# Performance work log

Measured on AMD Instinct MI355X. Metric: run time of the kernel, lower is better.

The kernel has to match this reference:

```python
import jax, jax.numpy as jnp
import numpy as np

S = 256          # seq_len
H = 1024         # hidden_size == input_size (required by inputs + hf add)
NUM_ITER = 1     # interaction module inner iterations
EPS = 1e-5       # BatchNorm1d eps


def setup_inputs() -> dict:
    key = jax.random.key(0)
    ks = jax.random.split(key, 16)
    xav = np.sqrt(2.0 / (H + H))          # xavier_normal for HxH dense
    u = 1.0 / np.sqrt(H)                  # torch LSTMCell default init scale
    inp = {"inputs": jax.random.normal(ks[0], (S, H), jnp.float32)}
    # interaction module dense layers
    for i in range(4):
        inp[f"W{i+1}"] = jax.random.normal(ks[1 + i], (H, H), jnp.float32) * xav
        inp[f"b{i+1}"] = jnp.zeros((H,), jnp.float32)
    # LSTM cells (forward / backward)
    inp["Wih_f"] = jax.random.uniform(ks[5], (4 * H, H), jnp.float32, -u, u)
    inp["Whh_f"] = jax.random.uniform(ks[6], (4 * H, H), jnp.float32, -u, u)
    inp["bih_f"] = jax.random.uniform(ks[7], (4 * H,), jnp.float32, -u, u)
    inp["bhh_f"] = jax.random.uniform(ks[8], (4 * H,), jnp.float32, -u, u)
    inp["Wih_b"] = jax.random.uniform(ks[9], (4 * H, H), jnp.float32, -u, u)
    inp["Whh_b"] = jax.random.uniform(ks[10], (4 * H, H), jnp.float32, -u, u)
    inp["bih_b"] = jax.random.uniform(ks[11], (4 * H,), jnp.float32, -u, u)
    inp["bhh_b"] = jax.random.uniform(ks[12], (4 * H,), jnp.float32, -u, u)
    # BatchNorm1d affine params (default init)
    inp["gamma_f"] = jnp.ones((H,), jnp.float32)
    inp["beta_f"] = jnp.zeros((H,), jnp.float32)
    inp["gamma_b"] = jnp.ones((H,), jnp.float32)
    inp["beta_b"] = jnp.zeros((H,), jnp.float32)
    return inp


def _bn(x, g, b):
    # training-mode BatchNorm1d over the batch (seq) axis, biased variance
    m = jnp.mean(x, axis=0)
    xc = x - m
    v = jnp.mean(xc * xc, axis=0)
    return xc * jax.lax.rsqrt(v + EPS) * g + b


def _lstm_c(x, h, c, Wih, Whh, bih, bhh):
    # torch LSTMCell: returns new cell state only (as used by the module)
    g = x @ Wih.T + bih + h @ Whh.T + bhh
    i, f, gg, o = jnp.split(g, 4)
    return jax.nn.sigmoid(f) * c + jax.nn.sigmoid(i) * jnp.tanh(gg)


def reference(inputs, W1, b1, W2, b2, W3, b3, W4, b4,
              Wih_f, Whh_f, bih_f, bhh_f, Wih_b, Whh_b, bih_b, bhh_b,
              gamma_f, beta_f, gamma_b, beta_b):
    sig = jax.nn.sigmoid

    def interaction(x0, hf, hb):
        for _ in range(NUM_ITER):
            x1 = sig((x0 + hf) @ W1.T + b1)
            hb2 = sig((hb + x1) @ W2.T + b2)
            hf2 = sig((x1 + hf) @ W3.T + b3)
            x0 = sig((hb2 + x1) @ W4.T + b4)
            hf, hb = hf2, hb2
        return x0, hf, hb

    def step(carry, t):
        hf, hb, fc, bc = carry
        _, hf2, hb2 = interaction(inputs, hf, hb)
        out = (hf2 + hb2) * 0.5  # value returned at the last timestep (pre-BN)
        tb = S - 1 - t
        fc = fc.at[t].set(_lstm_c(inputs[t], hf2[t], fc[t], Wih_f, Whh_f, bih_f, bhh_f))
        bc = bc.at[tb].set(_lstm_c(inputs[tb], hb2[tb], bc[tb], Wih_b, Whh_b, bih_b, bhh_b))
        hf_n = _bn(hf2, gamma_f, beta_f)
        hb_n = _bn(hb2, gamma_b, beta_b)
        return (hf_n, hb_n, fc, bc), out

    z = jnp.zeros((S, H), jnp.float32)
    (_, _, _, _), outs = jax.lax.scan(step, (z, z, z, z), jnp.arange(S))
    return outs[-1]  # [S, H]
```

## Files before the change

kernel.cpp:

```cpp
#include <hip/hip_runtime.h>
#include <hip/hip_bf16.h>
#include <math.h>

#define S 256
#define H 1024
#define SH (S*H)
#define EPS 1e-5f

typedef float f32x4 __attribute__((ext_vector_type(4)));
typedef short bf16x8 __attribute__((ext_vector_type(8)));

__device__ __forceinline__ float sigm(float x){ return 1.0f/(1.0f+expf(-x)); }

__device__ __forceinline__ ushort f2bf(float a){
    union { __hip_bfloat16 b; ushort u; } cv;
    cv.b = __float2bfloat16(a);
    return cv.u;
}
__device__ __forceinline__ float bf2f(ushort u){
    union { __hip_bfloat16 b; ushort u; } cv; cv.u = u;
    return __bfloat162float(cv.b);
}

__device__ __forceinline__ int xcd_swizzle(unsigned gbx) {
    return (int)((gbx & 7u) * 32u + (gbx >> 3));
}

__global__ __launch_bounds__(256) void k_pack(const float* __restrict__ W,
                                              ushort* __restrict__ ph,
                                              ushort* __restrict__ pl) {
    int p  = blockIdx.x * 256 + threadIdx.x;
    int l  = p & 63;
    int kt = (p >> 6) & 31;
    int jt = p >> 11;
    int j  = jt * 16 + (l & 15);
    int k0 = kt * 32 + ((l >> 4) << 3);
    const float* src = W + j * H + k0;
    float4 a0 = *(const float4*)src;
    float4 a1 = *(const float4*)(src + 4);
    float av[8] = {a0.x,a0.y,a0.z,a0.w,a1.x,a1.y,a1.z,a1.w};
    bf16x8 vh, vl;
#pragma unroll
    for (int e = 0; e < 8; ++e) {
        ushort h = f2bf(av[e]);
        vh[e] = (short)h;
        vl[e] = (short)f2bf(av[e] - bf2f(h));
    }
    *(bf16x8*)(ph + (size_t)p * 8) = vh;
    *(bf16x8*)(pl + (size_t)p * 8) = vl;
}

__global__ __launch_bounds__(256) void k_gemm1(
    const float* __restrict__ X,
    const ushort* __restrict__ Wph, const ushort* __restrict__ Wpl,
    const float* __restrict__ b1v,
    const float* __restrict__ rawF, const float* __restrict__ rawB,
    const float* __restrict__ statPrev,
    const float* __restrict__ gF, const float* __restrict__ bF,
    const float* __restrict__ gB, const float* __restrict__ bB,
    float* __restrict__ A2, float* __restrict__ A3,
    float* __restrict__ statz, int first)
{
    __shared__ __align__(16) ushort lhs_hi[8192];
    __shared__ __align__(16) ushort lhs_lo[8192];
    __shared__ float scF[H], ofF[H];

    int t = threadIdx.x;
    if (blockIdx.x < 16) statz[blockIdx.x * 256 + t] = 0.0f;

    int g = xcd_swizzle(blockIdx.x);
    int sb = g & 7, jb = g >> 3;
    int lane = t & 63, w = t >> 6;
    int wr = w >> 1, wc = w & 1;
    int row0 = sb * 32;
    int jt = jb * 2 + wc;
    const float inv = 1.0f / (float)S;

    if (!first) {
        for (int k = t; k < H; k += 256) {
            float m = statPrev[k] * inv;
            float v = statPrev[H + k] * inv - m * m;
            float sc = rsqrtf(v + EPS) * gF[k];
            scF[k] = sc;
            ofF[k] = bF[k] - m * sc;
        }
    }
    __syncthreads();

    f32x4 acc0 = {0,0,0,0}, acc1 = {0,0,0,0}, acc2 = {0,0,0,0};

    for (int phase = 0; phase < 4; ++phase) {
        int kbase = phase << 8;
#pragma unroll
        for (int it = 0; it < 4; ++it) {
            int gg = t + (it << 8);
            int s  = gg & 31;
            int kg = gg >> 5;
            int k  = kbase + (kg << 3);
            const float* xp = X + (row0 + s) * H + k;
            float4 x0 = *(const float4*)xp;
            float4 x1 = *(const float4*)(xp + 4);
            float a[8] = {x0.x,x0.y,x0.z,x0.w,x1.x,x1.y,x1.z,x1.w};
            if (!first) {
                const float* rp = rawF + (row0 + s) * H + k;
                float4 r0 = *(const float4*)rp;
                float4 r1 = *(const float4*)(rp + 4);
                float rr[8] = {r0.x,r0.y,r0.z,r0.w,r1.x,r1.y,r1.z,r1.w};
#pragma unroll
                for (int e = 0; e < 8; ++e)
                    a[e] += rr[e] * scF[k + e] + ofF[k + e];
            }
            bf16x8 vh, vl;
#pragma unroll
            for (int e = 0; e < 8; ++e) {
                ushort h = f2bf(a[e]);
                vh[e] = (short)h;
                vl[e] = (short)f2bf(a[e] - bf2f(h));
            }
            int st2 = s >> 4, q = kg & 3, kc = kg >> 2;
            int idx = (((st2 * 8 + kc) * 64) + ((q << 4) | (s & 15))) * 8;
            *(bf16x8*)(lhs_hi + idx) = vh;
            *(bf16x8*)(lhs_lo + idx) = vl;
        }
        __syncthreads();
        const ushort* bph = Wph + ((size_t)(jt * 32 + (phase << 3)) * 64 + lane) * 8;
        const ushort* bpl = Wpl + ((size_t)(jt * 32 + (phase << 3)) * 64 + lane) * 8;
        const ushort* ah  = lhs_hi + ((wr * 8) * 64 + lane) * 8;
        const ushort* al  = lhs_lo + ((wr * 8) * 64 + lane) * 8;
#pragma unroll
        for (int kc = 0; kc < 8; ++kc) {
            bf16x8 a_h = *(const bf16x8*)(ah + kc * 512);
            bf16x8 a_l = *(const bf16x8*)(al + kc * 512);
            bf16x8 b_h = *(const bf16x8*)(bph + kc * 512);
            bf16x8 b_l = *(const bf16x8*)(bpl + kc * 512);
            acc0 = __builtin_amdgcn_mfma_f32_16x16x32_bf16(a_h, b_h, acc0, 0, 0, 0);
            acc1 = __builtin_amdgcn_mfma_f32_16x16x32_bf16(a_h, b_l, acc1, 0, 0, 0);
            acc2 = __builtin_amdgcn_mfma_f32_16x16x32_bf16(a_l, b_h, acc2, 0, 0, 0);
        }
        __syncthreads();
    }

    int j = jt * 16 + (lane & 15);
    int srow = row0 + wr * 16 + ((lane >> 4) << 2);
    float bias = b1v[j];
    float scFj = 0.f, ofFj = 0.f, scBj = 0.f, ofBj = 0.f;
    if (!first) {
        scFj = scF[j]; ofFj = ofF[j];
        float m = statPrev[2 * H + j] * inv;
        float v = statPrev[3 * H + j] * inv - m * m;
        scBj = rsqrtf(v + EPS) * gB[j];
        ofBj = bB[j] - m * scBj;
    }
    f32x4 sum = acc0 + acc1 + acc2;
#pragma unroll
    for (int r = 0; r < 4; ++r) {
        int o = (srow + r) * H + j;
        float x1v = sigm(sum[r] + bias);
        float hb_ = first ? 0.f : rawB[o] * scBj + ofBj;
        float hf_ = first ? 0.f : rawF[o] * scFj + ofFj;
        A2[o] = hb_ + x1v;
        A3[o] = x1v + hf_;
    }
}

__global__ __launch_bounds__(256) void k_gemm23(
    const float* __restrict__ A2g, const float* __restrict__ A3g,
    const ushort* __restrict__ W2h, const ushort* __restrict__ W2l,
    const ushort* __restrict__ W3h, const ushort* __restrict__ W3l,
    const float* __restrict__ b2v, const float* __restrict__ b3v,
    float* __restrict__ rawF, float* __restrict__ rawB,
    float* __restrict__ stats, float* __restrict__ outp, int writeOut)
{
    __shared__ __align__(16) ushort lhs_hi[8192];
    __shared__ __align__(16) ushort lhs_lo[8192];
    __shared__ float red[4][64][2];

    int t = threadIdx.x;
    int g = xcd_swizzle(blockIdx.x);
    int sb = g & 7, jb = g >> 3;
    int lane = t & 63, w = t >> 6;
    int wr = w >> 1, wc = w & 1;
    int row0 = sb * 32;
    int jt = jb * 2 + wc;
    int j = jt * 16 + (lane & 15);
    int srow = row0 + wr * 16 + ((lane >> 4) << 2);

    float vb[4];

    {
        f32x4 acc0 = {0,0,0,0}, acc1 = {0,0,0,0}, acc2 = {0,0,0,0};
        for (int phase = 0; phase < 4; ++phase) {
            int kbase = phase << 8;
#pragma unroll
            for (int it = 0; it < 4; ++it) {
                int gg = t + (it << 8);
                int s = gg & 31, kg = gg >> 5;
                int k = kbase + (kg << 3);
                const float* xp = A2g + (row0 + s) * H + k;
                float4 x0 = *(const float4*)xp;
                float4 x1 = *(const float4*)(xp + 4);
                float a[8] = {x0.x,x0.y,x0.z,x0.w,x1.x,x1.y,x1.z,x1.w};
                bf16x8 vh, vl;
#pragma unroll
                for (int e = 0; e < 8; ++e) {
                    ushort h = f2bf(a[e]);
                    vh[e] = (short)h;
                    vl[e] = (short)f2bf(a[e] - bf2f(h));
                }
                int idx = ((((s >> 4) * 8 + (kg >> 2)) * 64) + (((kg & 3) << 4) | (s & 15))) * 8;
                *(bf16x8*)(lhs_hi + idx) = vh;
                *(bf16x8*)(lhs_lo + idx) = vl;
            }
            __syncthreads();
            const ushort* bph = W2h + ((size_t)(jt * 32 + (phase << 3)) * 64 + lane) * 8;
            const ushort* bpl = W2l + ((size_t)(jt * 32 + (phase << 3)) * 64 + lane) * 8;
            const ushort* ah  = lhs_hi + ((wr * 8) * 64 + lane) * 8;
            const ushort* al  = lhs_lo + ((wr * 8) * 64 + lane) * 8;
#pragma unroll
            for (int kc = 0; kc < 8; ++kc) {
                bf16x8 a_h = *(const bf16x8*)(ah + kc * 512);
                bf16x8 a_l = *(const bf16x8*)(al + kc * 512);
                bf16x8 b_h = *(const bf16x8*)(bph + kc * 512);
                bf16x8 b_l = *(const bf16x8*)(bpl + kc * 512);
                acc0 = __builtin_amdgcn_mfma_f32_16x16x32_bf16(a_h, b_h, acc0, 0, 0, 0);
                acc1 = __builtin_amdgcn_mfma_f32_16x16x32_bf16(a_h, b_l, acc1, 0, 0, 0);
                acc2 = __builtin_amdgcn_mfma_f32_16x16x32_bf16(a_l, b_h, acc2, 0, 0, 0);
            }
            __syncthreads();
        }
        f32x4 sum = acc0 + acc1 + acc2;
        float bias = b2v[j];
        float ts = 0.f, tq = 0.f;
#pragma unroll
        for (int r = 0; r < 4; ++r) {
            float v = sigm(sum[r] + bias);
            vb[r] = v;
            rawB[(srow + r) * H + j] = v;
            ts += v; tq += v * v;
        }
        red[w][lane][0] = ts;
        red[w][lane][1] = tq;
    }
    __syncthreads();
    if (t < 32) {
        int wc2 = t >> 4, jl = t & 15;
        int jj = jb * 32 + wc2 * 16 + jl;
        float ts = 0.f, tq = 0.f;
#pragma unroll
        for (int wr2 = 0; wr2 < 2; ++wr2)
#pragma unroll
            for (int lg = 0; lg < 4; ++lg) {
                ts += red[wr2 * 2 + wc2][lg * 16 + jl][0];
                tq += red[wr2 * 2 + wc2][lg * 16 + jl][1];
            }
        atomicAdd(&stats[2 * H + jj], ts);
        atomicAdd(&stats[3 * H + jj], tq);
    }

    {
        f32x4 acc0 = {0,0,0,0}, acc1 = {0,0,0,0}, acc2 = {0,0,0,0};
        for (int phase = 0; phase < 4; ++phase) {
            int kbase = phase << 8;
            __syncthreads();
#pragma unroll
            for (int it = 0; it < 4; ++it) {
                int gg = t + (it << 8);
                int s = gg & 31, kg = gg >> 5;
                int k = kbase + (kg << 3);
                const float* xp = A3g + (row0 + s) * H + k;
                float4 x0 = *(const float4*)xp;
                float4 x1 = *(const float4*)(xp + 4);
                float a[8] = {x0.x,x0.y,x0.z,x0.w,x1.x,x1.y,x1.z,x1.w};
                bf16x8 vh, vl;
#pragma unroll
                for (int e = 0; e < 8; ++e) {
                    ushort h = f2bf(a[e]);
                    vh[e] = (short)h;
                    vl[e] = (short)f2bf(a[e] - bf2f(h));
                }
                int idx = ((((s >> 4) * 8 + (kg >> 2)) * 64) + (((kg & 3) << 4) | (s & 15))) * 8;
                *(bf16x8*)(lhs_hi + idx) = vh;
                *(bf16x8*)(lhs_lo + idx) = vl;
            }
            __syncthreads();
            const ushort* bph = W3h + ((size_t)(jt * 32 + (phase << 3)) * 64 + lane) * 8;
            const ushort* bpl = W3l + ((size_t)(jt * 32 + (phase << 3)) * 64 + lane) * 8;
            const ushort* ah  = lhs_hi + ((wr * 8) * 64 + lane) * 8;
            const ushort* al  = lhs_lo + ((wr * 8) * 64 + lane) * 8;
#pragma unroll
            for (int kc = 0; kc < 8; ++kc) {
                bf16x8 a_h = *(const bf16x8*)(ah + kc * 512);
                bf16x8 a_l = *(const bf16x8*)(al + kc * 512);
                bf16x8 b_h = *(const bf16x8*)(bph + kc * 512);
                bf16x8 b_l = *(const bf16x8*)(bpl + kc * 512);
                acc0 = __builtin_amdgcn_mfma_f32_16x16x32_bf16(a_h, b_h, acc0, 0, 0, 0);
                acc1 = __builtin_amdgcn_mfma_f32_16x16x32_bf16(a_h, b_l, acc1, 0, 0, 0);
                acc2 = __builtin_amdgcn_mfma_f32_16x16x32_bf16(a_l, b_h, acc2, 0, 0, 0);
            }
        }
        __syncthreads();
        f32x4 sum = acc0 + acc1 + acc2;
        float bias = b3v[j];
        float ts = 0.f, tq = 0.f;
#pragma unroll
        for (int r = 0; r < 4; ++r) {
            float v = sigm(sum[r] + bias);
            rawF[(srow + r) * H + j] = v;
            if (writeOut)
                outp[(srow + r) * H + j] = 0.5f * (v + vb[r]);
            ts += v; tq += v * v;
        }
        red[w][lane][0] = ts;
        red[w][lane][1] = tq;
    }
    __syncthreads();
    if (t < 32) {
        int wc2 = t >> 4, jl = t & 15;
        int jj = jb * 32 + wc2 * 16 + jl;
        float ts = 0.f, tq = 0.f;
#pragma unroll
        for (int wr2 = 0; wr2 < 2; ++wr2)
#pragma unroll
            for (int lg = 0; lg < 4; ++lg) {
                ts += red[wr2 * 2 + wc2][lg * 16 + jl][0];
                tq += red[wr2 * 2 + wc2][lg * 16 + jl][1];
            }
        atomicAdd(&stats[0 * H + jj], ts);
        atomicAdd(&stats[1 * H + jj], tq);
    }
}

extern "C" void kernel_launch(void* const* d_in, const int* in_sizes, int n_in,
                              void* d_out, int out_size, void* d_ws, size_t ws_size,
                              hipStream_t stream) {
    (void)in_sizes; (void)n_in; (void)out_size; (void)ws_size;

    const float* X  = (const float*)d_in[0];
    const float* W1 = (const float*)d_in[1];
    const float* b1 = (const float*)d_in[2];
    const float* W2 = (const float*)d_in[3];
    const float* b2 = (const float*)d_in[4];
    const float* W3 = (const float*)d_in[5];
    const float* b3 = (const float*)d_in[6];
    const float* gf = (const float*)d_in[17];
    const float* bf = (const float*)d_in[18];
    const float* gb = (const float*)d_in[19];
    const float* bb = (const float*)d_in[20];

    char* base = (char*)d_ws;
    const size_t MB = 1024 * 1024;
    ushort* wp1h = (ushort*)(base + 0 * MB);
    ushort* wp1l = (ushort*)(base + 2 * MB);
    ushort* wp2h = (ushort*)(base + 4 * MB);
    ushort* wp2l = (ushort*)(base + 6 * MB);
    ushort* wp3h = (ushort*)(base + 8 * MB);
    ushort* wp3l = (ushort*)(base + 10 * MB);
    float*  A2   = (float*)(base + 12 * MB);
    float*  A3   = (float*)(base + 13 * MB);
    float*  rawf = (float*)(base + 14 * MB);
    float*  rawb = (float*)(base + 16 * MB);
    float*  stats= (float*)(base + 18 * MB);

    k_pack<<<512, 256, 0, stream>>>(W1, wp1h, wp1l);
    k_pack<<<512, 256, 0, stream>>>(W2, wp2h, wp2l);
    k_pack<<<512, 256, 0, stream>>>(W3, wp3h, wp3l);

    for (int s = 0; s < S; ++s) {
        int p = (s + 1) & 1;
        int q = s & 1;
        k_gemm1<<<256, 256, 0, stream>>>(
            X, wp1h, wp1l, b1,
            rawf + q * SH, rawb + q * SH, stats + q * 4 * H,
            gf, bf, gb, bb,
            A2, A3, stats + p * 4 * H, (s == 0) ? 1 : 0);
        k_gemm23<<<256, 256, 0, stream>>>(
            A2, A3, wp2h, wp2l, wp3h, wp3l, b2, b3,
            rawf + p * SH, rawb + p * SH, stats + p * 4 * H,
            (float*)d_out, (s == S - 1) ? 1 : 0);
    }
}
```

Before: 14.97 ms.

## Fuse per-step kernels into one persistent kernel with software grid barriers

```diff
diff --git a/kernel.cpp b/kernel.cpp
--- a/kernel.cpp
+++ b/kernel.cpp
@@ -50,283 +50,272 @@
     *(bf16x8*)(pl + (size_t)p * 8) = vl;
 }
 
-__global__ __launch_bounds__(256) void k_gemm1(
+__global__ __launch_bounds__(256) void k_init(float* __restrict__ stats,
+                                              unsigned* __restrict__ sync) {
+    int t = blockIdx.x * 256 + threadIdx.x;
+    if (t < 8 * H) stats[t] = 0.0f;
+    if (t == 0) { sync[0] = 0u; sync[64] = 0u; }
+}
+
+__device__ __forceinline__ void grid_barrier(unsigned* ctrp, unsigned* flagp,
+                                             unsigned want) {
+    __syncthreads();
+    if (threadIdx.x == 0) {
+        __threadfence();
+        unsigned old = __hip_atomic_fetch_add(ctrp, 1u, __ATOMIC_RELAXED,
+                                              __HIP_MEMORY_SCOPE_AGENT);
+        if (old == want * 256u - 1u) {
+            __hip_atomic_store(flagp, want, __ATOMIC_RELEASE,
+                               __HIP_MEMORY_SCOPE_AGENT);
+        } else {
+            while (__hip_atomic_load(flagp, __ATOMIC_RELAXED,
+                                     __HIP_MEMORY_SCOPE_AGENT) < want)
+                __builtin_amdgcn_s_sleep(1);
+        }
+        __threadfence();
+    }
+    __syncthreads();
+}
+
+__global__ __launch_bounds__(256) void k_persist(
     const float* __restrict__ X,
-    const ushort* __restrict__ Wph, const ushort* __restrict__ Wpl,
-    const float* __restrict__ b1v,
-    const float* __restrict__ rawF, const float* __restrict__ rawB,
-    const float* __restrict__ statPrev,
-    const float* __restrict__ gF, const float* __restrict__ bF,
-    const float* __restrict__ gB, const float* __restrict__ bB,
-    float* __restrict__ A2, float* __restrict__ A3,
-    float* __restrict__ statz, int first)
+    const ushort* __restrict__ wp1h, const ushort* __restrict__ wp1l,
+    const ushort* __restrict__ wp2h, const ushort* __restrict__ wp2l,
+    const ushort* __restrict__ wp3h, const ushort* __restrict__ wp3l,
+    const float* __restrict__ b1v, const float* __restrict__ b2v,
+    const float* __restrict__ b3v,
+    const float* __restrict__ gFv, const float* __restrict__ bFv,
+    const float* __restrict__ gBv, const float* __restrict__ bBv,
+    ushort* __restrict__ A2h, ushort* __restrict__ A2l,
+    ushort* __restrict__ A3h, ushort* __restrict__ A3l,
+    float* __restrict__ rawf, float* __restrict__ rawb,
+    float* __restrict__ stats, float* __restrict__ outp,
+    unsigned* __restrict__ syncv)
 {
     __shared__ __align__(16) ushort lhs_hi[8192];
     __shared__ __align__(16) ushort lhs_lo[8192];
     __shared__ float scF[H], ofF[H];
-
-    int t = threadIdx.x;
-    if (blockIdx.x < 16) statz[blockIdx.x * 256 + t] = 0.0f;
-
-    int g = xcd_swizzle(blockIdx.x);
-    int sb = g & 7, jb = g >> 3;
-    int lane = t & 63, w = t >> 6;
-    int wr = w >> 1, wc = w & 1;
-    int row0 = sb * 32;
-    int jt = jb * 2 + wc;
+    __shared__ float red[4][64][2];
+
+    const int t = threadIdx.x;
+    const int g = xcd_swizzle(blockIdx.x);
+    const int sb = g & 7, jb = g >> 3;
+    const int lane = t & 63, w = t >> 6;
+    const int wr = w >> 1, wc = w & 1;
+    const int row0 = sb * 32;
+    const int jt = jb * 2 + wc;
+    const int j = jt * 16 + (lane & 15);
+    const int arow = row0 + wr * 16 + (lane & 15);
+    const int koff = (lane >> 4) << 3;
+    const int srow = row0 + wr * 16 + ((lane >> 4) << 2);
     const float inv = 1.0f / (float)S;
 
-    if (!first) {
-        for (int k = t; k < H; k += 256) {
-            float m = statPrev[k] * inv;
-            float v = statPrev[H + k] * inv - m * m;
-            float sc = rsqrtf(v + EPS) * gF[k];
-            scF[k] = sc;
-            ofF[k] = bF[k] - m * sc;
-        }
-    }
-    __syncthreads();
-
-    f32x4 acc0 = {0,0,0,0}, acc1 = {0,0,0,0}, acc2 = {0,0,0,0};
-
-    for (int phase = 0; phase < 4; ++phase) {
-        int kbase = phase << 8;
-#pragma unroll
-        for (int it = 0; it < 4; ++it) {
-            int gg = t + (it << 8);
-            int s  = gg & 31;
-            int kg = gg >> 5;
-            int k  = kbase + (kg << 3);
-            const float* xp = X + (row0 + s) * H + k;
-            float4 x0 = *(const float4*)xp;
-            float4 x1 = *(const float4*)(xp + 4);
-            float a[8] = {x0.x,x0.y,x0.z,x0.w,x1.x,x1.y,x1.z,x1.w};
+    unsigned* ctrp  = syncv;
+    unsigned* flagp = syncv + 64;
+    unsigned bgen = 0;
+
+    for (int s = 0; s < S; ++s) {
+        const int p = (s + 1) & 1, q = s & 1;
+        const int first = (s == 0);
+        const float* stP = stats + q * 4 * H;
+        float* stA = stats + p * 4 * H;
+        const float* rF = rawf + q * SH;
+        const float* rB = rawb + q * SH;
+        float* wF = rawf + p * SH;
+        float* wB = rawb + p * SH;
+
+        if (!first) {
+            for (int k = t; k < H; k += 256) {
+                float m = stP[k] * inv;
+                float v = stP[H + k] * inv - m * m;
+                float sc = rsqrtf(v + EPS) * gFv[k];
+                scF[k] = sc;
+                ofF[k] = bFv[k] - m * sc;
+            }
+        }
+        __syncthreads();
+
+        {
+            f32x4 acc0 = {0,0,0,0}, acc1 = {0,0,0,0}, acc2 = {0,0,0,0};
+            for (int phase = 0; phase < 4; ++phase) {
+                int kbase = phase << 8;
+#pragma unroll
+                for (int it = 0; it < 4; ++it) {
+                    int gg = t + (it << 8);
+                    int si = gg & 31, kg = gg >> 5;
+                    int k = kbase + (kg << 3);
+                    const float* xp = X + (row0 + si) * H + k;
+                    float4 x0 = *(const float4*)xp;
+                    float4 x1 = *(const float4*)(xp + 4);
+                    float a[8] = {x0.x,x0.y,x0.z,x0.w,x1.x,x1.y,x1.z,x1.w};
+                    if (!first) {
+                        const float* rp = rF + (row0 + si) * H + k;
+                        float4 r0 = *(const float4*)rp;
+                        float4 r1 = *(const float4*)(rp + 4);
+                        float rr[8] = {r0.x,r0.y,r0.z,r0.w,r1.x,r1.y,r1.z,r1.w};
+#pragma unroll
+                        for (int e = 0; e < 8; ++e)
+                            a[e] += rr[e] * scF[k + e] + ofF[k + e];
+                    }
+                    bf16x8 vh, vl;
+#pragma unroll
+                    for (int e = 0; e < 8; ++e) {
+                        ushort h = f2bf(a[e]);
+                        vh[e] = (short)h;
+                        vl[e] = (short)f2bf(a[e] - bf2f(h));
+                    }
+                    int idx = ((((si >> 4) * 8 + (kg >> 2)) * 64) +
+                               (((kg & 3) << 4) | (si & 15))) * 8;
+                    *(bf16x8*)(lhs_hi + idx) = vh;
+                    *(bf16x8*)(lhs_lo + idx) = vl;
+                }
+                __syncthreads();
+                const ushort* bph = wp1h + ((size_t)(jt * 32 + (phase << 3)) * 64 + lane) * 8;
+                const ushort* bpl = wp1l + ((size_t)(jt * 32 + (phase << 3)) * 64 + lane) * 8;
+                const ushort* ah  = lhs_hi + ((wr * 8) * 64 + lane) * 8;
+                const ushort* al  = lhs_lo + ((wr * 8) * 64 + lane) * 8;
+#pragma unroll
+                for (int kc = 0; kc < 8; ++kc) {
+                    bf16x8 a_h = *(const bf16x8*)(ah + kc * 512);
+                    bf16x8 a_l = *(const bf16x8*)(al + kc * 512);
+                    bf16x8 b_h = *(const bf16x8*)(bph + kc * 512);
+                    bf16x8 b_l = *(const bf16x8*)(bpl + kc * 512);
+                    acc0 = __builtin_amdgcn_mfma_f32_16x16x32_bf16(a_h, b_h, acc0, 0, 0, 0);
+                    acc1 = __builtin_amdgcn_mfma_f32_16x16x32_bf16(a_h, b_l, acc1, 0, 0, 0);
+                    acc2 = __builtin_amdgcn_mfma_f32_16x16x32_bf16(a_l, b_h, acc2, 0, 0, 0);
+                }
+                __syncthreads();
+            }
+
+            float bias = b1v[j];
+            float scFj = 0.f, ofFj = 0.f, scBj = 0.f, ofBj = 0.f;
             if (!first) {
-                const float* rp = rawF + (row0 + s) * H + k;
-                float4 r0 = *(const float4*)rp;
-                float4 r1 = *(const float4*)(rp + 4);
-                float rr[8] = {r0.x,r0.y,r0.z,r0.w,r1.x,r1.y,r1.z,r1.w};
-#pragma unroll
-                for (int e = 0; e < 8; ++e)
-                    a[e] += rr[e] * scF[k + e] + ofF[k + e];
-            }
-            bf16x8 vh, vl;
-#pragma unroll
-            for (int e = 0; e < 8; ++e) {
-                ushort h = f2bf(a[e]);
-                vh[e] = (short)h;
-                vl[e] = (short)f2bf(a[e] - bf2f(h));
-            }
-            int st2 = s >> 4, q = kg & 3, kc = kg >> 2;
-            int idx = (((st2 * 8 + kc) * 64) + ((q << 4) | (s & 15))) * 8;
-            *(bf16x8*)(lhs_hi + idx) = vh;
-            *(bf16x8*)(lhs_lo + idx) = vl;
+                scFj = scF[j]; ofFj = ofF[j];
+                float m = stP[2 * H + j] * inv;
+                float v = stP[3 * H + j] * inv - m * m;
+                scBj = rsqrtf(v + EPS) * gBv[j];
+                ofBj = bBv[j] - m * scBj;
+            }
+            f32x4 sum = acc0 + acc1 + acc2;
+#pragma unroll
+            for (int r = 0; r < 4; ++r) {
+                int o = (srow + r) * H + j;
+                float x1v = sigm(sum[r] + bias);
+                float hb_ = first ? 0.f : rB[o] * scBj + ofBj;
+                float hf_ = first ? 0.f : rF[o] * scFj + ofFj;
+                float a2 = hb_ + x1v;
+                float a3 = x1v + hf_;
+                ushort h2 = f2bf(a2);
+                A2h[o] = h2;
+                A2l[o] = f2bf(a2 - bf2f(h2));
+                ushort h3 = f2bf(a3);
+                A3h[o] = h3;
+                A3l[o] = f2bf(a3 - bf2f(h3));
+            }
+        }
+
+        grid_barrier(ctrp, flagp, ++bgen);
+
+        if (blockIdx.x == 0) {
+            float* z = stats + q * 4 * H;
+            for (int k = t; k < 4 * H; k += 256) z[k] = 0.0f;
+        }
+
+        float vb[4];
+        {
+            f32x4 acc0 = {0,0,0,0}, acc1 = {0,0,0,0}, acc2 = {0,0,0,0};
+            const ushort* ah = A2h + arow * H + koff;
+            const ushort* al = A2l + arow * H + koff;
+            const ushort* bh = wp2h + ((size_t)(jt * 32) * 64 + lane) * 8;
+            const ushort* bl = wp2l + ((size_t)(jt * 32) * 64 + lane) * 8;
+#pragma unroll 8
+            for (int kc = 0; kc < 32; ++kc) {
+                bf16x8 vah = *(const bf16x8*)(ah + kc * 32);
+                bf16x8 val = *(const bf16x8*)(al + kc * 32);
+                bf16x8 vbh = *(const bf16x8*)(bh + kc * 512);
+                bf16x8 vbl = *(const bf16x8*)(bl + kc * 512);
+                acc0 = __builtin_amdgcn_mfma_f32_16x16x32_bf16(vah, vbh, acc0, 0, 0, 0);
+                acc1 = __builtin_amdgcn_mfma_f32_16x16x32_bf16(vah, vbl, acc1, 0, 0, 0);
+                acc2 = __builtin_amdgcn_mfma_f32_16x16x32_bf16(val, vbh, acc2, 0, 0, 0);
+            }
+            f32x4 sum = acc0 + acc1 + acc2;
+            float bias = b2v[j];
+            float ts = 0.f, tq = 0.f;
+#pragma unroll
+            for (int r = 0; r < 4; ++r) {
+                float v = sigm(sum[r] + bias);
+                vb[r] = v;
+                wB[(srow + r) * H + j] = v;
+                ts += v; tq += v * v;
+            }
+            red[w][lane][0] = ts;
+            red[w][lane][1] = tq;
         }
         __syncthreads();
-        const ushort* bph = Wph + ((size_t)(jt * 32 + (phase << 3)) * 64 + lane) * 8;
-        const ushort* bpl = Wpl + ((size_t)(jt * 32 + (phase << 3)) * 64 + lane) * 8;
-        const ushort* ah  = lhs_hi + ((wr * 8) * 64 + lane) * 8;
-        const ushort* al  = lhs_lo + ((wr * 8) * 64 + lane) * 8;
-#pragma unroll
-        for (int kc = 0; kc < 8; ++kc) {
-            bf16x8 a_h = *(const bf16x8*)(ah + kc * 512);
-            bf16x8 a_l = *(const bf16x8*)(al + kc * 512);
-            bf16x8 b_h = *(const bf16x8*)(bph + kc * 512);
-            bf16x8 b_l = *(const bf16x8*)(bpl + kc * 512);
-            acc0 = __builtin_amdgcn_mfma_f32_16x16x32_bf16(a_h, b_h, acc0, 0, 0, 0);
-            acc1 = __builtin_amdgcn_mfma_f32_16x16x32_bf16(a_h, b_l, acc1, 0, 0, 0);
-            acc2 = __builtin_amdgcn_mfma_f32_16x16x32_bf16(a_l, b_h, acc2, 0, 0, 0);
+        if (t < 32) {
+            int wc2 = t >> 4, jl = t & 15;
+            int jj = jb * 32 + wc2 * 16 + jl;
+            float ts = 0.f, tq = 0.f;
+#pragma unroll
+            for (int wr2 = 0; wr2 < 2; ++wr2)
+#pragma unroll
+                for (int lg = 0; lg < 4; ++lg) {
+                    ts += red[wr2 * 2 + wc2][lg * 16 + jl][0];
+                    tq += red[wr2 * 2 + wc2][lg * 16 + jl][1];
+                }
+            atomicAdd(&stA[2 * H + jj], ts);
+            atomicAdd(&stA[3 * H + jj], tq);
         }
         __syncthreads();
-    }
-
-    int j = jt * 16 + (lane & 15);
-    int srow = row0 + wr * 16 + ((lane >> 4) << 2);
-    float bias = b1v[j];
-    float scFj = 0.f, ofFj = 0.f, scBj = 0.f, ofBj = 0.f;
-    if (!first) {
-        scFj = scF[j]; ofFj = ofF[j];
-        float m = statPrev[2 * H + j] * inv;
-        float v = statPrev[3 * H + j] * inv - m * m;
-        scBj = rsqrtf(v + EPS) * gB[j];
-        ofBj = bB[j] - m * scBj;
-    }
-    f32x4 sum = acc0 + acc1 + acc2;
-#pragma unroll
-    for (int r = 0; r < 4; ++r) {
-        int o = (srow + r) * H + j;
-        float x1v = sigm(sum[r] + bias);
-        float hb_ = first ? 0.f : rawB[o] * scBj + ofBj;
-        float hf_ = first ? 0.f : rawF[o] * scFj + ofFj;
-        A2[o] = hb_ + x1v;
-        A3[o] = x1v + hf_;
-    }
-}
-
-__global__ __launch_bounds__(256) void k_gemm23(
-    const float* __restrict__ A2g, const float* __restrict__ A3g,
-    const ushort* __restrict__ W2h, const ushort* __restrict__ W2l,
-    const ushort* __restrict__ W3h, const ushort* __restrict__ W3l,
-    const float* __restrict__ b2v, const float* __restrict__ b3v,
-    float* __restrict__ rawF, float* __restrict__ rawB,
-    float* __restrict__ stats, float* __restrict__ outp, int writeOut)
-{
-    __shared__ __align__(16) ushort lhs_hi[8192];
-    __shared__ __align__(16) ushort lhs_lo[8192];
-    __shared__ float red[4][64][2];
-
-    int t = threadIdx.x;
-    int g = xcd_swizzle(blockIdx.x);
-    int sb = g & 7, jb = g >> 3;
-    int lane = t & 63, w = t >> 6;
-    int wr = w >> 1, wc = w & 1;
-    int row0 = sb * 32;
-    int jt = jb * 2 + wc;
-    int j = jt * 16 + (lane & 15);
-    int srow = row0 + wr * 16 + ((lane >> 4) << 2);
-
-    float vb[4];
-
-    {
-        f32x4 acc0 = {0,0,0,0}, acc1 = {0,0,0,0}, acc2 = {0,0,0,0};
-        for (int phase = 0; phase < 4; ++phase) {
-            int kbase = phase << 8;
-#pragma unroll
-            for (int it = 0; it < 4; ++it) {
-                int gg = t + (it << 8);
-                int s = gg & 31, kg = gg >> 5;
-                int k = kbase + (kg << 3);
-                const float* xp = A2g + (row0 + s) * H + k;
-                float4 x0 = *(const float4*)xp;
-                float4 x1 = *(const float4*)(xp + 4);
-                float a[8] = {x0.x,x0.y,x0.z,x0.w,x1.x,x1.y,x1.z,x1.w};
-                bf16x8 vh, vl;
-#pragma unroll
-                for (int e = 0; e < 8; ++e) {
-                    ushort h = f2bf(a[e]);
-                    vh[e] = (short)h;
-                    vl[e] = (short)f2bf(a[e] - bf2f(h));
+
+        {
+            f32x4 acc0 = {0,0,0,0}, acc1 = {0,0,0,0}, acc2 = {0,0,0,0};
+            const ushort* ah = A3h + arow * H + koff;
+            const ushort* al = A3l + arow * H + koff;
+            const ushort* bh = wp3h + ((size_t)(jt * 32) * 64 + lane) * 8;
+            const ushort* bl = wp3l + ((size_t)(jt * 32) * 64 + lane) * 8;
+#pragma unroll 8
+            for (int kc = 0; kc < 32; ++kc) {
+                bf16x8 vah = *(const bf16x8*)(ah + kc * 32);
+                bf16x8 val = *(const bf16x8*)(al + kc * 32);
+                bf16x8 vbh = *(const bf16x8*)(bh + kc * 512);
+                bf16x8 vbl = *(const bf16x8*)(bl + kc * 512);
+                acc0 = __builtin_amdgcn_mfma_f32_16x16x32_bf16(vah, vbh, acc0, 0, 0, 0);
+                acc1 = __builtin_amdgcn_mfma_f32_16x16x32_bf16(vah, vbl, acc1, 0, 0, 0);
+                acc2 = __builtin_amdgcn_mfma_f32_16x16x32_bf16(val, vbh, acc2, 0, 0, 0);
+            }
+            f32x4 sum = acc0 + acc1 + acc2;
+            float bias = b3v[j];
+            float ts = 0.f, tq = 0.f;
+#pragma unroll
+            for (int r = 0; r < 4; ++r) {
+                float v = sigm(sum[r] + bias);
+                wF[(srow + r) * H + j] = v;
+                if (s == S - 1)
+                    outp[(srow + r) * H + j] = 0.5f * (v + vb[r]);
+                ts += v; tq += v * v;
+            }
+            red[w][lane][0] = ts;
+            red[w][lane][1] = tq;
+        }
+        __syncthreads();
+        if (t < 32) {
+            int wc2 = t >> 4, jl = t & 15;
+            int jj = jb * 32 + wc2 * 16 + jl;
+            float ts = 0.f, tq = 0.f;
+#pragma unroll
+            for (int wr2 = 0; wr2 < 2; ++wr2)
+#pragma unroll
+                for (int lg = 0; lg < 4; ++lg) {
+                    ts += red[wr2 * 2 + wc2][lg * 16 + jl][0];
+                    tq += red[wr2 * 2 + wc2][lg * 16 + jl][1];
                 }
-                int idx = ((((s >> 4) * 8 + (kg >> 2)) * 64) + (((kg & 3) << 4) | (s & 15))) * 8;
-                *(bf16x8*)(lhs_hi + idx) = vh;
-                *(bf16x8*)(lhs_lo + idx) = vl;
-            }
-            __syncthreads();
-            const ushort* bph = W2h + ((size_t)(jt * 32 + (phase << 3)) * 64 + lane) * 8;
-            const ushort* bpl = W2l + ((size_t)(jt * 32 + (phase << 3)) * 64 + lane) * 8;
-            const ushort* ah  = lhs_hi + ((wr * 8) * 64 + lane) * 8;
-            const ushort* al  = lhs_lo + ((wr * 8) * 64 + lane) * 8;
-#pragma unroll
-            for (int kc = 0; kc < 8; ++kc) {
-                bf16x8 a_h = *(const bf16x8*)(ah + kc * 512);
-                bf16x8 a_l = *(const bf16x8*)(al + kc * 512);
-                bf16x8 b_h = *(const bf16x8*)(bph + kc * 512);
-                bf16x8 b_l = *(const bf16x8*)(bpl + kc * 512);
-                acc0 = __builtin_amdgcn_mfma_f32_16x16x32_bf16(a_h, b_h, acc0, 0, 0, 0);
-                acc1 = __builtin_amdgcn_mfma_f32_16x16x32_bf16(a_h, b_l, acc1, 0, 0, 0);
-                acc2 = __builtin_amdgcn_mfma_f32_16x16x32_bf16(a_l, b_h, acc2, 0, 0, 0);
-            }
-            __syncthreads();
-        }
-        f32x4 sum = acc0 + acc1 + acc2;
-        float bias = b2v[j];
-        float ts = 0.f, tq = 0.f;
-#pragma unroll
-        for (int r = 0; r < 4; ++r) {
-            float v = sigm(sum[r] + bias);
-            vb[r] = v;
-            rawB[(srow + r) * H + j] = v;
-            ts += v; tq += v * v;
-        }
-        red[w][lane][0] = ts;
-        red[w][lane][1] = tq;
-    }
-    __syncthreads();
-    if (t < 32) {
-        int wc2 = t >> 4, jl = t & 15;
-        int jj = jb * 32 + wc2 * 16 + jl;
-        float ts = 0.f, tq = 0.f;
-#pragma unroll
-        for (int wr2 = 0; wr2 < 2; ++wr2)
-#pragma unroll
-            for (int lg = 0; lg < 4; ++lg) {
-                ts += red[wr2 * 2 + wc2][lg * 16 + jl][0];
-                tq += red[wr2 * 2 + wc2][lg * 16 + jl][1];
-            }
-        atomicAdd(&stats[2 * H + jj], ts);
-        atomicAdd(&stats[3 * H + jj], tq);
-    }
-
-    {
-        f32x4 acc0 = {0,0,0,0}, acc1 = {0,0,0,0}, acc2 = {0,0,0,0};
-        for (int phase = 0; phase < 4; ++phase) {
-            int kbase = phase << 8;
-            __syncthreads();
-#pragma unroll
-            for (int it = 0; it < 4; ++it) {
-                int gg = t + (it << 8);
-                int s = gg & 31, kg = gg >> 5;
-                int k = kbase + (kg << 3);
-                const float* xp = A3g + (row0 + s) * H + k;
-                float4 x0 = *(const float4*)xp;
-                float4 x1 = *(const float4*)(xp + 4);
-                float a[8] = {x0.x,x0.y,x0.z,x0.w,x1.x,x1.y,x1.z,x1.w};
-                bf16x8 vh, vl;
-#pragma unroll
-                for (int e = 0; e < 8; ++e) {
-                    ushort h = f2bf(a[e]);
-                    vh[e] = (short)h;
-                    vl[e] = (short)f2bf(a[e] - bf2f(h));
-                }
-                int idx = ((((s >> 4) * 8 + (kg >> 2)) * 64) + (((kg & 3) << 4) | (s & 15))) * 8;
-                *(bf16x8*)(lhs_hi + idx) = vh;
-                *(bf16x8*)(lhs_lo + idx) = vl;
-            }
-            __syncthreads();
-            const ushort* bph = W3h + ((size_t)(jt * 32 + (phase << 3)) * 64 + lane) * 8;
-            const ushort* bpl = W3l + ((size_t)(jt * 32 + (phase << 3)) * 64 + lane) * 8;
-            const ushort* ah  = lhs_hi + ((wr * 8) * 64 + lane) * 8;
-            const ushort* al  = lhs_lo + ((wr * 8) * 64 + lane) * 8;
-#pragma unroll
-            for (int kc = 0; kc < 8; ++kc) {
-                bf16x8 a_h = *(const bf16x8*)(ah + kc * 512);
-                bf16x8 a_l = *(const bf16x8*)(al + kc * 512);
-                bf16x8 b_h = *(const bf16x8*)(bph + kc * 512);
-                bf16x8 b_l = *(const bf16x8*)(bpl + kc * 512);
-                acc0 = __builtin_amdgcn_mfma_f32_16x16x32_bf16(a_h, b_h, acc0, 0, 0, 0);
-                acc1 = __builtin_amdgcn_mfma_f32_16x16x32_bf16(a_h, b_l, acc1, 0, 0, 0);
-                acc2 = __builtin_amdgcn_mfma_f32_16x16x32_bf16(a_l, b_h, acc2, 0, 0, 0);
-            }
-        }
-        __syncthreads();
-        f32x4 sum = acc0 + acc1 + acc2;
-        float bias = b3v[j];
-        float ts = 0.f, tq = 0.f;
-#pragma unroll
-        for (int r = 0; r < 4; ++r) {
-            float v = sigm(sum[r] + bias);
-            rawF[(srow + r) * H + j] = v;
-            if (writeOut)
-                outp[(srow + r) * H + j] = 0.5f * (v + vb[r]);
-            ts += v; tq += v * v;
-        }
-        red[w][lane][0] = ts;
-        red[w][lane][1] = tq;
-    }
-    __syncthreads();
-    if (t < 32) {
-        int wc2 = t >> 4, jl = t & 15;
-        int jj = jb * 32 + wc2 * 16 + jl;
-        float ts = 0.f, tq = 0.f;
-#pragma unroll
-        for (int wr2 = 0; wr2 < 2; ++wr2)
-#pragma unroll
-            for (int lg = 0; lg < 4; ++lg) {
-                ts += red[wr2 * 2 + wc2][lg * 16 + jl][0];
-                tq += red[wr2 * 2 + wc2][lg * 16 + jl][1];
-            }
-        atomicAdd(&stats[0 * H + jj], ts);
-        atomicAdd(&stats[1 * H + jj], tq);
+            atomicAdd(&stA[0 * H + jj], ts);
+            atomicAdd(&stA[1 * H + jj], tq);
+        }
+
+        if (s != S - 1)
+            grid_barrier(ctrp, flagp, ++bgen);
     }
 }
 
@@ -355,27 +344,23 @@
     ushort* wp2l = (ushort*)(base + 6 * MB);
     ushort* wp3h = (ushort*)(base + 8 * MB);
     ushort* wp3l = (ushort*)(base + 10 * MB);
-    float*  A2   = (float*)(base + 12 * MB);
-    float*  A3   = (float*)(base + 13 * MB);
+    ushort* A2h  = (ushort*)(base + 12 * MB);
+    ushort* A2l  = (ushort*)(base + 12 * MB + 512 * 1024);
+    ushort* A3h  = (ushort*)(base + 13 * MB);
+    ushort* A3l  = (ushort*)(base + 13 * MB + 512 * 1024);
     float*  rawf = (float*)(base + 14 * MB);
     float*  rawb = (float*)(base + 16 * MB);
     float*  stats= (float*)(base + 18 * MB);
+    unsigned* syncv = (unsigned*)(base + 18 * MB + 64 * 1024);
 
     k_pack<<<512, 256, 0, stream>>>(W1, wp1h, wp1l);
     k_pack<<<512, 256, 0, stream>>>(W2, wp2h, wp2l);
     k_pack<<<512, 256, 0, stream>>>(W3, wp3h, wp3l);
-
-    for (int s = 0; s < S; ++s) {
-        int p = (s + 1) & 1;
-        int q = s & 1;
-        k_gemm1<<<256, 256, 0, stream>>>(
-            X, wp1h, wp1l, b1,
-            rawf + q * SH, rawb + q * SH, stats + q * 4 * H,
-            gf, bf, gb, bb,
-            A2, A3, stats + p * 4 * H, (s == 0) ? 1 : 0);
-        k_gemm23<<<256, 256, 0, stream>>>(
-            A2, A3, wp2h, wp2l, wp3h, wp3l, b2, b3,
-            rawf + p * SH, rawb + p * SH, stats + p * 4 * H,
-            (float*)d_out, (s == S - 1) ? 1 : 0);
-    }
-}
+    k_init<<<33, 256, 0, stream>>>(stats, syncv);
+
+    k_persist<<<256, 256, 0, stream>>>(
+        X, wp1h, wp1l, wp2h, wp2l, wp3h, wp3l,
+        b1, b2, b3, gf, bf, gb, bb,
+        A2h, A2l, A3h, A3l,
+        rawf, rawb, stats, (float*)d_out, syncv);
+}
```

Result: slower. 16.51 ms (+10.3%).
